# Kernel tuning notes

Hardware: AMD Instinct MI355X
Metric: run time of the kernel (lower is better)

Reference implementation:

```python
import jax, jax.numpy as jnp
import numpy as np

N, E = 20000, 100000
F_IN, F_OUT = 1024, 512
NUM_FILT = 8
DIM = 3  # output_dim per coordinate-function type (4 types -> 12 total)


def _death_indices(f, edge_index):
    """0-dim persistence pairing via union-find over a vertex filtration.
    Returns death[v]: index of the node whose filtration value kills the
    component created by v (death[v] == v for unpaired/essential nodes)."""
    u, v = edge_index[0], edge_index[1]
    fu, fv = f[u], f[v]
    d_idx = jnp.where(fu >= fv, u, v)          # node realizing the edge value max(f[u], f[v])
    order = jnp.argsort(jnp.maximum(fu, fv))   # process edges in increasing filtration order
    edges = jnp.stack([u[order], v[order], d_idx[order]], axis=1)  # [E, 3]
    n = f.shape[0]

    def find(parent, i):
        return jax.lax.while_loop(lambda j: parent[j] != j, lambda j: parent[j], i)

    def step(carry, e):
        parent, death = carry
        ra = find(parent, e[0])
        rb = find(parent, e[1])
        older = jnp.where(f[ra] <= f[rb], ra, rb)   # older (smaller birth) component survives
        younger = ra + rb - older                   # the other root dies at this edge
        merge = ra != rb
        parent = jnp.where(merge, parent.at[younger].set(older), parent)
        death = jnp.where(merge, death.at[younger].set(e[2]), death)
        return (parent, death), None

    idx = jnp.arange(n)
    (_, death), _ = jax.lax.scan(step, (idx, idx), edges)
    return death


def _coord_activations(p, tri_t, gauss_mu, gauss_sigma, line_w, rhat_c, rhat_r):
    """p: [N, 2] persistence pairs -> [N, 4*DIM] coordinate-function features."""
    b, d = p[:, 0:1], p[:, 1:2]
    tri = jax.nn.relu(d - jnp.abs(tri_t[None, :] - b))                     # Triangle_transform
    diff = p[:, None, :] - gauss_mu[None, :, :]
    gauss = jnp.exp(-jnp.sum(diff * diff, -1) / (2.0 * gauss_sigma ** 2))  # Gaussian_transform
    line = p @ line_w.T                                                    # Line_transform
    q = jnp.sum(jnp.abs(p[:, None, :] - rhat_c[None, :, :]), -1)
    rhat = 1.0 / (1.0 + q) - 1.0 / (1.0 + jnp.abs(jnp.abs(rhat_r) - q))    # RationalHat_transform
    return jnp.concatenate([tri, gauss, line, rhat], axis=1)


def _forward(x, filt_w, filt_b, tri_t, gauss_mu, gauss_sigma, line_w,
             rhat_c, rhat_r, out_w, out_b, edge_index):
    f_all = (x @ filt_w.T + filt_b).T                     # [NUM_FILT, N] filtration values
    f_sg = jax.lax.stop_gradient(f_all)                   # pairing structure is combinatorial
    death = jax.vmap(lambda ff: _death_indices(ff, edge_index))(f_sg)  # [NUM_FILT, N] int
    pairs = jnp.stack([f_all, jnp.take_along_axis(f_all, death, axis=1)], axis=-1)  # [F, N, 2]
    acts = jax.vmap(lambda p: _coord_activations(p, tri_t, gauss_mu, gauss_sigma,
                                                 line_w, rhat_c, rhat_r))(pairs)  # [F, N, 12]
    coord = jnp.transpose(acts, (1, 0, 2)).reshape(x.shape[0], -1)  # torch.cat over filtrations
    return jnp.concatenate([x, coord], axis=1) @ out_w.T + out_b


def setup_inputs() -> dict:
    key = jax.random.key(0)
    ks = jax.random.split(key, 10)
    s = 0.02
    return {
        "x": jax.random.normal(ks[0], (N, F_IN), jnp.float32),
        "edge_index": jax.random.randint(ks[1], (2, E), 0, N),
        "filt_w": jax.random.normal(ks[2], (NUM_FILT, F_IN), jnp.float32) * s,
        "filt_b": jnp.zeros((NUM_FILT,), jnp.float32),
        "tri_t": jax.random.normal(ks[3], (DIM,), jnp.float32),
        "gauss_mu": jax.random.normal(ks[4], (DIM, 2), jnp.float32),
        "gauss_sigma": jnp.asarray(0.5, jnp.float32),
        "line_w": jax.random.normal(ks[5], (DIM, 2), jnp.float32),
        "rhat_c": jax.random.normal(ks[6], (DIM, 2), jnp.float32),
        "rhat_r": jnp.asarray(1.0, jnp.float32),
        "out_w": jax.random.normal(ks[7], (F_OUT, F_IN + NUM_FILT * 4 * DIM), jnp.float32) * s,
        "out_b": jnp.zeros((F_OUT,), jnp.float32),
    }


def reference(x, edge_index, filt_w, filt_b, tri_t, gauss_mu, gauss_sigma,
              line_w, rhat_c, rhat_r, out_w, out_b):
    return _forward(x, filt_w, filt_b, tri_t, gauss_mu, gauss_sigma,
                    line_w, rhat_c, rhat_r, out_w, out_b, edge_index)
```

## Files before the change

### kernel.cpp

```cpp
#include <hip/hip_runtime.h>
#include <stdint.h>

#define NV 20000
#define NE 100000
#define NK 8
#define FIN 1024
#define FOUT 512
#define FTOT 1120
#define KP 1152
#define MP 20096
#define CAP 4096
#define ROUNDS 13
#define NB 32
#define CHUNK (NE / NB)
#define LDA 72

typedef unsigned int u32;
typedef unsigned long long u64;
typedef unsigned short u16;
typedef __attribute__((ext_vector_type(8))) short bf16x8;
typedef __attribute__((ext_vector_type(4))) float f32x4;

__device__ __forceinline__ u32 sb(float x) {
    u32 u = __float_as_uint(x);
    return u ^ ((u & 0x80000000u) ? 0xFFFFFFFFu : 0x80000000u);
}
__device__ __forceinline__ float isb(u32 s) {
    u32 u = (s & 0x80000000u) ? (s ^ 0x80000000u) : ~s;
    return __uint_as_float(u);
}
__device__ __forceinline__ u16 f2bf(float f) {
    u32 u = __float_as_uint(f);
    return (u16)((u + 0x7FFFu + ((u >> 16) & 1u)) >> 16);
}

__global__ __launch_bounds__(256) void k_fx(
    const float* __restrict__ x, const float* __restrict__ fw,
    const float* __restrict__ fb, float* __restrict__ f, u16* __restrict__ A) {
    __shared__ float w[NK * FIN];
    __shared__ float xs[4][FIN];
    for (int i = threadIdx.x; i < NK * FIN; i += 256) w[i] = fw[i];
    __syncthreads();
    int wave = threadIdx.x >> 6, lane = threadIdx.x & 63;
    int v = blockIdx.x * 4 + wave;
    float4* xd = (float4*)xs[wave];
    if (v < NV) {
        const float4* xr4 = (const float4*)(x + (size_t)v * FIN);
        for (int i = lane; i < FIN / 4; i += 64) xd[i] = xr4[i];
    } else {
        for (int i = lane; i < FIN / 4; i += 64) xd[i] = make_float4(0.f, 0.f, 0.f, 0.f);
    }
    float acc[NK];
#pragma unroll
    for (int k = 0; k < NK; k++) acc[k] = 0.f;
    for (int c = 0; c < FIN / 64; c++) {
        int i = c * 64 + lane;
        float xv = xs[wave][i];
#pragma unroll
        for (int k = 0; k < NK; k++) acc[k] = fmaf(xv, w[k * FIN + i], acc[k]);
    }
#pragma unroll
    for (int off = 32; off >= 1; off >>= 1)
#pragma unroll
        for (int k = 0; k < NK; k++) acc[k] += __shfl_xor(acc[k], off, 64);
    if (v < NV && lane < NK) f[lane * NV + v] = acc[lane] + fb[lane];
    for (int cc = lane; cc < 144; cc += 64) {
        int c0 = cc * 8;
        u32 pk[4];
        if (c0 < FIN) {
#pragma unroll
            for (int j = 0; j < 4; j++)
                pk[j] = (u32)f2bf(xs[wave][c0 + 2 * j]) |
                        ((u32)f2bf(xs[wave][c0 + 2 * j + 1]) << 16);
        } else {
#pragma unroll
            for (int j = 0; j < 4; j++) pk[j] = 0u;
        }
        *(uint4*)(A + (size_t)v * KP + c0) = make_uint4(pk[0], pk[1], pk[2], pk[3]);
    }
}

__global__ void k_init(u32* __restrict__ comp, u64* __restrict__ cand, u32* cnts) {
    int t = blockIdx.x * 256 + threadIdx.x;
    comp[t] = (u32)(t % CAP);
    cand[t] = ~0ull;
    if (t < 32) cnts[t] = 0;
}

__global__ void k_castw(const float* __restrict__ ow, u16* __restrict__ W) {
    int t = blockIdx.x * 256 + threadIdx.x;
    if (t >= FOUT * 144) return;
    int n = t / 144, c = (t % 144) * 8;
    u32 pk[4];
    if (c < FTOT) {
        const float* wr = ow + (size_t)n * FTOT + c;
#pragma unroll
        for (int j = 0; j < 4; j++)
            pk[j] = (u32)f2bf(wr[2 * j]) | ((u32)f2bf(wr[2 * j + 1]) << 16);
    } else {
#pragma unroll
        for (int j = 0; j < 4; j++) pk[j] = 0u;
    }
    *(uint4*)(W + (size_t)n * KP + c) = make_uint4(pk[0], pk[1], pk[2], pk[3]);
}

__global__ void k_initdesc(const float* __restrict__ f, u64* __restrict__ cd,
                           float* __restrict__ dval) {
    int t = blockIdx.x * 256 + threadIdx.x;
    u32 v = (u32)(t % NV);
    float fv = f[t];
    cd[t] = ((u64)sb(fv) << 32) | v;
    dval[t] = fv;
}

__global__ void k_descedge(const int* __restrict__ ei, const float* __restrict__ f,
                           u64* __restrict__ cd) {
    int t = blockIdx.x * 256 + threadIdx.x;
    int k = t / NE, e = t % NE;
    int a = ei[e], b = ei[NE + e];
    if (a == b) return;
    float fa = f[k * NV + a], fb2 = f[k * NV + b];
    int d, l; float fl;
    if (fa >= fb2) { d = a; l = b; fl = fb2; } else { d = b; l = a; fl = fa; }
    u64 key = ((u64)sb(fl) << 32) | (u32)l;
    atomicMin(&cd[k * NV + d], key);
}

__global__ __launch_bounds__(1024) void k_basmin(
    const u64* __restrict__ cd, u32* __restrict__ basin,
    u32* nmin, u32* __restrict__ mlist, u32* __restrict__ dense) {
    __shared__ u32 nxt[NV];
    __shared__ u32 changed;
    int k = blockIdx.x;
    const u64* c = cd + (size_t)k * NV;
    for (int i = threadIdx.x; i < NV; i += 1024) nxt[i] = (u32)c[i];
    if (threadIdx.x == 0) changed = 0u;
    __syncthreads();
    for (int pass = 0; pass < 16; pass++) {
        bool ch = false;
        for (int i = threadIdx.x; i < NV; i += 1024) {
            u32 a = nxt[i];
            u32 b = nxt[a];
            if (b != a) {
                u32 c2 = nxt[b];
                u32 d2 = nxt[c2];
                nxt[i] = d2;
                ch = true;
            }
        }
        if (ch) changed = 1u;
        __syncthreads();
        u32 done = (changed == 0u);
        __syncthreads();
        if (threadIdx.x == 0) changed = 0u;
        __syncthreads();
        if (done) break;
    }
    for (int i = threadIdx.x; i < NV; i += 1024) {
        u32 r = nxt[i];
        basin[k * NV + i] = r;
        if (r == (u32)i) {
            u32 id = atomicAdd(&nmin[k], 1u);
            if (id < CAP) { mlist[k * CAP + id] = (u32)i; dense[k * NV + i] = id; }
        }
    }
}

__global__ void k_edgeprep(const int* __restrict__ ei, const float* __restrict__ f,
                           const u32* __restrict__ basin, const u32* __restrict__ dense,
                           u64* __restrict__ wkey, u32* __restrict__ ep) {
    int t = blockIdx.x * 256 + threadIdx.x;
    int k = t / NE, e = t % NE;
    int a = ei[e], b = ei[NE + e];
    if (a == b) { ep[t] = 0xFFFFFFFFu; return; }
    float fa = f[k * NV + a], fb2 = f[k * NV + b];
    float w = (fa >= fb2) ? fa : fb2;
    wkey[t] = ((u64)sb(w) << 32) | (u32)e;
    u32 ba = basin[k * NV + a], bb = basin[k * NV + b];
    if (ba == bb) { ep[t] = 0xFFFFFFFFu; return; }
    u32 da = dense[k * NV + ba], db = dense[k * NV + bb];
    ep[t] = (da << 16) | db;
}

__device__ __forceinline__ u32 rootofs(const u32* c, u32 i) {
    while (true) { u32 p = c[i]; if (p == i) return i; i = p; }
}

__global__ void k_candA(const u32* __restrict__ ep, const u64* __restrict__ wkey,
                        const u32* __restrict__ comp_g, u64* __restrict__ cand_g,
                        const u32* __restrict__ done) {
    __shared__ u32 scomp[CAP];
    __shared__ u64 scand[CAP];
    int k = blockIdx.y, b = blockIdx.x;
    if (done[k]) return;
    for (int i = threadIdx.x; i < CAP; i += 256) {
        scomp[i] = comp_g[k * CAP + i];
        scand[i] = ~0ull;
    }
    __syncthreads();
    int e0 = b * CHUNK;
    const u32* epk = ep + (size_t)k * NE;
    const u64* wkk = wkey + (size_t)k * NE;
    for (int e = e0 + threadIdx.x; e < e0 + CHUNK; e += 256) {
        u32 p32 = epk[e];
        if (p32 == 0xFFFFFFFFu) continue;
        u32 A = rootofs(scomp, p32 >> 16), B = rootofs(scomp, p32 & 0xFFFFu);
        if (A == B) continue;
        u64 w = wkk[e];
        atomicMin(&scand[A], w);
        atomicMin(&scand[B], w);
    }
    __syncthreads();
    u64* cnd = cand_g + (size_t)k * CAP;
    for (int i = threadIdx.x; i < CAP; i += 256) {
        u64 v = scand[i];
        if (v != ~0ull) atomicMin(&cnd[i], v);
    }
}

__global__ void k_round(u64* __restrict__ cand_g, const u32* __restrict__ ep,
                        u32* __restrict__ comp_g, u32* mstcnt,
                        u64* __restrict__ mkey, u32* __restrict__ done) {
    __shared__ u64 scand[CAP];
    __shared__ u32 scomp[CAP];
    __shared__ u32 shk[CAP];
    __shared__ u32 nmerge;
    int k = blockIdx.x;
    if (done[k]) return;
    if (threadIdx.x == 0) nmerge = 0;
    for (int i = threadIdx.x; i < CAP; i += 1024) {
        scand[i] = cand_g[k * CAP + i];
        scomp[i] = comp_g[k * CAP + i];
    }
    __syncthreads();
    for (int i = threadIdx.x; i < CAP; i += 1024) {
        u64 cc = scand[i];
        if (cc == ~0ull) { shk[i] = (u32)i; continue; }
        u32 e = (u32)cc;
        u32 p32 = ep[(size_t)k * NE + e];
        u32 A = rootofs(scomp, p32 >> 16), B = rootofs(scomp, p32 & 0xFFFFu);
        shk[i] = (A == (u32)i) ? B : A;
    }
    __syncthreads();
    for (int i = threadIdx.x; i < CAP; i += 1024) {
        u32 o = shk[i];
        if (o == (u32)i) continue;
        bool mutual = (shk[o] == (u32)i);
        if (mutual && (u32)i < o) continue;
        scomp[i] = o;
        u64 cc = scand[i];
        u32 j = atomicAdd(&mstcnt[k], 1u);
        atomicAdd(&nmerge, 1u);
        if (j < CAP) mkey[k * CAP + j] = cc;
    }
    __syncthreads();
    for (int i = threadIdx.x; i < CAP; i += 1024) scomp[i] = rootofs(scomp, i);
    __syncthreads();
    for (int i = threadIdx.x; i < CAP; i += 1024) {
        comp_g[k * CAP + i] = scomp[i];
        cand_g[k * CAP + i] = ~0ull;
    }
    if (threadIdx.x == 0 && nmerge == 0) done[k] = 1;
}

__global__ __launch_bounds__(1024) void k_sort(const u32* mstcnt, u64* __restrict__ mkey) {
    __shared__ u64 skey[CAP];
    int k = blockIdx.x;
    u32 cnt = mstcnt[k]; if (cnt > CAP) cnt = CAP;
    int n2 = 64; while (n2 < (int)cnt) n2 <<= 1;
    for (int i = threadIdx.x; i < n2; i += 1024)
        skey[i] = (i < (int)cnt) ? mkey[k * CAP + i] : ~0ull;
    __syncthreads();
    int half = n2 >> 1;
    for (int sz = 2; sz <= n2; sz <<= 1) {
        for (int st = sz >> 1; st >= 1; st >>= 1) {
            for (int t = threadIdx.x; t < half; t += 1024) {
                int i = ((t & ~(st - 1)) << 1) | (t & (st - 1));
                int j = i | st;
                bool up = ((i & sz) == 0);
                u64 a = skey[i], b = skey[j];
                if (up ? (a > b) : (a < b)) { skey[i] = b; skey[j] = a; }
            }
            __syncthreads();
        }
    }
    for (int i = threadIdx.x; i < (int)cnt; i += 1024)
        mkey[k * CAP + i] = skey[i];
}

__global__ __launch_bounds__(64) void k_pairw(
    const u32* nmin, const u32* __restrict__ mlist, const u32* mstcnt,
    const u64* __restrict__ mkey, const u32* __restrict__ ep,
    const float* __restrict__ f, float* __restrict__ dval) {
    __shared__ u32 par[CAP];
    __shared__ u32 val[CAP];
    __shared__ u32 tag[CAP];
    int k = blockIdx.x;
    int lane = threadIdx.x;
    u32 nm = nmin[k]; if (nm > CAP) nm = CAP;
    u32 cnt = mstcnt[k]; if (cnt > CAP) cnt = CAP;
    for (int i = lane; i < CAP; i += 64) {
        par[i] = (u32)i;
        tag[i] = 0u;
        val[i] = (i < (int)nm) ? __float_as_uint(f[k * NV + mlist[k * CAP + i]]) : 0u;
    }
    __syncthreads();
    u32 nw = (cnt + 63) >> 6;
    u64 nkey = 0; u32 npay = 0;
    if ((u32)lane < cnt) {
        nkey = mkey[(size_t)k * CAP + lane];
        npay = ep[(size_t)k * NE + (u32)nkey];
    }
    for (u32 w = 0; w < nw; w++) {
        u64 key = nkey; u32 pay = npay;
        bool valid = (w * 64 + (u32)lane) < cnt;
        u32 jn = (w + 1) * 64 + (u32)lane;
        if (jn < cnt) {
            nkey = mkey[(size_t)k * CAP + jn];
            npay = ep[(size_t)k * NE + (u32)nkey];
        }
        u32 wb = (u32)(key >> 32);
        u32 la = pay >> 16, lb = pay & 0xFFFFu;
        u32 rA = la, rB = lb;
        if (valid) {
            while (true) {
                u32 pA = par[rA], pB = par[rB];
                bool dA = (pA == rA), dB = (pB == rB);
                if (dA && dB) break;
                if (!dA) { u32 g = par[pA]; par[rA] = g; rA = g; }
                if (!dB) { u32 g = par[pB]; par[rB] = g; rB = g; }
            }
        }
        u32 vA = valid ? val[rA] : 0u;
        u32 vB = valid ? val[rB] : 0u;
        if (valid) { atomicAdd(&tag[rA], 1u); atomicAdd(&tag[rB], 1u); }
        u32 cA = rA, cvA = vA, cB = rB, cvB = vB;
        u32 t_fy = 0xFFFFFFFFu, t_fo = 0u, t_fvo = 0u;
        if (valid) {
            if (__uint_as_float(cvA) <= __uint_as_float(cvB)) { t_fo = cA; t_fvo = cvA; t_fy = cB; }
            else                                              { t_fo = cB; t_fvo = cvB; t_fy = cA; }
        }
        u32 pkd = (t_fy << 16) | (t_fo & 0xFFFFu);
        bool pend = valid && (atomicAdd(&tag[t_fy], 0u) > 1u);
        u64 m = __ballot(pend);
        while (m) {
            u32 s = (u32)__builtin_ctzll(m);
            m &= m - 1;
            u32 opk = __builtin_amdgcn_readlane(pkd, (int)s);
            u32 ov  = __builtin_amdgcn_readlane(t_fvo, (int)s);
            u32 oy = opk >> 16, oo = opk & 0xFFFFu;
            if ((u32)lane == s) pend = false;
            bool app = valid && ((u32)lane > s);
            bool mA = app && (cA == oy);
            bool mB = app && (cB == oy);
            if (mA) { cA = oo; cvA = ov; }
            if (mB) { cB = oo; cvB = ov; }
            bool rm = mA || mB;
            if (__any(rm)) {
                if (rm) {
                    atomicAdd(&tag[oo], 1u);
                    if (__uint_as_float(cvA) <= __uint_as_float(cvB)) { t_fo = cA; t_fvo = cvA; t_fy = cB; }
                    else                                              { t_fo = cB; t_fvo = cvB; t_fy = cA; }
                    pkd = (t_fy << 16) | (t_fo & 0xFFFFu);
                    pend = atomicAdd(&tag[t_fy], 0u) > 1u;
                }
                m = __ballot(pend);
                m &= (s < 63u) ? (~0ull << (s + 1)) : 0ull;
            }
        }
        if (valid) { tag[rA] = 0u; tag[rB] = 0u; }
        if (valid) { par[t_fy] = t_fo; val[t_fy] = wb; }
        __syncthreads();
    }
    for (int i = lane; i < (int)nm; i += 64) {
        if (par[i] != (u32)i)
            dval[k * NV + mlist[k * CAP + i]] = isb(val[i]);
    }
}

__global__ void k_coordb(const float* __restrict__ f, const float* __restrict__ dval,
                         const float* __restrict__ tri_t, const float* __restrict__ gmu,
                         const float* __restrict__ gsig, const float* __restrict__ lw,
                         const float* __restrict__ rc, const float* __restrict__ rr,
                         u16* __restrict__ A) {
    int t = blockIdx.x * 256 + threadIdx.x;
    int k = t / NV, v = t % NV;
    float b = f[t], d = dval[t];
    float o[12];
    float s = gsig[0];
    float inv2s2 = 1.0f / (2.0f * s * s);
    float r = fabsf(rr[0]);
#pragma unroll
    for (int j = 0; j < 3; j++) {
        float tri = d - fabsf(tri_t[j] - b);
        o[j] = tri > 0.f ? tri : 0.f;
        float dx = b - gmu[2 * j], dy = d - gmu[2 * j + 1];
        o[3 + j] = expf(-(dx * dx + dy * dy) * inv2s2);
        o[6 + j] = b * lw[2 * j] + d * lw[2 * j + 1];
        float q = fabsf(b - rc[2 * j]) + fabsf(d - rc[2 * j + 1]);
        o[9 + j] = 1.0f / (1.0f + q) - 1.0f / (1.0f + fabsf(r - q));
    }
    u16* dst = A + (size_t)v * KP + FIN + k * 12;
    u32* d32 = (u32*)dst;
#pragma unroll
    for (int j = 0; j < 6; j++)
        d32[j] = (u32)f2bf(o[2 * j]) | ((u32)f2bf(o[2 * j + 1]) << 16);
}

__global__ __launch_bounds__(512, 2) void k_gemm2(
    const u16* __restrict__ A, const u16* __restrict__ W,
    const float* __restrict__ bias, float* __restrict__ out) {
    __shared__ u16 As[128 * LDA];
    __shared__ u16 Ws[512 * LDA];
    int m0 = blockIdx.x * 128;
    int t = threadIdx.x;
    int wave = t >> 6, lane = t & 63;
    int wr = wave >> 2, wc = wave & 3;
    int lrow = lane & 15, lq = lane >> 4;
    f32x4 acc[4][8];
#pragma unroll
    for (int mt = 0; mt < 4; mt++)
#pragma unroll
        for (int nt = 0; nt < 8; nt++) acc[mt][nt] = (f32x4){0.f, 0.f, 0.f, 0.f};

    int arow[2], acol[2], wrow[8], wcol[8];
    uint4 av[2], wv[8];
#pragma unroll
    for (int i = 0; i < 2; i++) {
        int c = i * 512 + t;
        arow[i] = c >> 3; acol[i] = (c & 7) * 8;
        av[i] = *(const uint4*)(A + (size_t)(m0 + arow[i]) * KP + acol[i]);
    }
#pragma unroll
    for (int i = 0; i < 8; i++) {
        int c = i * 512 + t;
        wrow[i] = c >> 3; wcol[i] = (c & 7) * 8;
        wv[i] = *(const uint4*)(W + (size_t)wrow[i] * KP + wcol[i]);
    }
#pragma unroll 1
    for (int step = 0; step < KP / 64; step++) {
        __syncthreads();
#pragma unroll
        for (int i = 0; i < 2; i++) *(uint4*)(As + arow[i] * LDA + acol[i]) = av[i];
#pragma unroll
        for (int i = 0; i < 8; i++) *(uint4*)(Ws + wrow[i] * LDA + wcol[i]) = wv[i];
        __syncthreads();
        int k0n = (step + 1 < KP / 64) ? (step + 1) * 64 : 0;
#pragma unroll
        for (int i = 0; i < 2; i++)
            av[i] = *(const uint4*)(A + (size_t)(m0 + arow[i]) * KP + k0n + acol[i]);
#pragma unroll
        for (int i = 0; i < 8; i++)
            wv[i] = *(const uint4*)(W + (size_t)wrow[i] * KP + k0n + wcol[i]);
#pragma unroll
        for (int kh = 0; kh < 2; kh++) {
            int kk = kh * 32 + lq * 8;
            bf16x8 af[4], wf[8];
#pragma unroll
            for (int mt = 0; mt < 4; mt++)
                af[mt] = *(const bf16x8*)(As + (wr * 64 + mt * 16 + lrow) * LDA + kk);
#pragma unroll
            for (int nt = 0; nt < 8; nt++)
                wf[nt] = *(const bf16x8*)(Ws + (wc * 128 + nt * 16 + lrow) * LDA + kk);
#pragma unroll
            for (int mt = 0; mt < 4; mt++)
#pragma unroll
                for (int nt = 0; nt < 8; nt++)
                    acc[mt][nt] = __builtin_amdgcn_mfma_f32_16x16x32_bf16(
                        af[mt], wf[nt], acc[mt][nt], 0, 0, 0);
        }
    }
    __syncthreads();
    float* scr = (float*)Ws + wave * 576;
    int cg = lane & 7;
    int rr8 = lane >> 3;
#pragma unroll
    for (int np = 0; np < 4; np++) {
        int o = wc * 128 + np * 32 + cg * 4;
        f32x4 b4 = *(const f32x4*)(bias + o);
#pragma unroll
        for (int mt = 0; mt < 4; mt++) {
#pragma unroll
            for (int fh = 0; fh < 2; fh++) {
                f32x4 fr = acc[mt][2 * np + fh];
#pragma unroll
                for (int i = 0; i < 4; i++)
                    scr[(lq * 4 + i) * 36 + fh * 16 + lrow] = fr[i];
            }
#pragma unroll
            for (int p = 0; p < 2; p++) {
                int r = p * 8 + rr8;
                f32x4 vv = *(f32x4*)(scr + r * 36 + cg * 4);
                int v = m0 + wr * 64 + mt * 16 + r;
                if (v < NV) *(f32x4*)(out + (size_t)v * FOUT + o) = vv + b4;
            }
        }
    }
}

extern "C" void kernel_launch(void* const* d_in, const int* in_sizes, int n_in,
                              void* d_out, int out_size, void* d_ws, size_t ws_size,
                              hipStream_t stream) {
    const float* x     = (const float*)d_in[0];
    const int*   ei    = (const int*)d_in[1];
    const float* fw    = (const float*)d_in[2];
    const float* fbv   = (const float*)d_in[3];
    const float* tri_t = (const float*)d_in[4];
    const float* gmu   = (const float*)d_in[5];
    const float* gsig  = (const float*)d_in[6];
    const float* lw    = (const float*)d_in[7];
    const float* rc    = (const float*)d_in[8];
    const float* rr    = (const float*)d_in[9];
    const float* ow    = (const float*)d_in[10];
    const float* ob    = (const float*)d_in[11];
    float* out = (float*)d_out;

    char* p = (char*)d_ws;
    auto alloc = [&](size_t bytes) -> void* {
        void* q = (void*)p;
        p += (bytes + 255) & ~(size_t)255;
        return q;
    };
    float* f     = (float*)alloc((size_t)NK * NV * 4);
    u64*   cd    = (u64*)  alloc((size_t)NK * NV * 8);
    u32*   basin = (u32*)  alloc((size_t)NK * NV * 4);
    u32*   dense = (u32*)  alloc((size_t)NK * NV * 4);
    u32*   mlist = (u32*)  alloc((size_t)NK * CAP * 4);
    u32*   cnts  = (u32*)  alloc(64 * 4);
    u64*   wkey  = (u64*)  alloc((size_t)NK * NE * 8);
    u32*   ep    = (u32*)  alloc((size_t)NK * NE * 4);
    u32*   comp  = (u32*)  alloc((size_t)NK * CAP * 4);
    u64*   cand  = (u64*)  alloc((size_t)NK * CAP * 8);
    u64*   mkey  = (u64*)  alloc((size_t)NK * CAP * 8);
    float* dval  = (float*)alloc((size_t)NK * NV * 4);
    u16*   Ab    = (u16*)  alloc((size_t)MP * KP * 2);
    u16*   Wb    = (u16*)  alloc((size_t)FOUT * KP * 2);
    u32* nmin = cnts; u32* mstcnt = cnts + 8; u32* done = cnts + 16;

    k_init<<<128, 256, 0, stream>>>(comp, cand, cnts);
    k_fx<<<MP / 4, 256, 0, stream>>>(x, fw, fbv, f, Ab);
    k_castw<<<(FOUT * 144 + 255) / 256, 256, 0, stream>>>(ow, Wb);
    k_initdesc<<<625, 256, 0, stream>>>(f, cd, dval);
    k_descedge<<<3125, 256, 0, stream>>>(ei, f, cd);
    k_basmin<<<NK, 1024, 0, stream>>>(cd, basin, nmin, mlist, dense);
    k_edgeprep<<<3125, 256, 0, stream>>>(ei, f, basin, dense, wkey, ep);
    for (int r = 0; r < ROUNDS; r++) {
        k_candA<<<dim3(NB, NK), 256, 0, stream>>>(ep, wkey, comp, cand, done);
        k_round<<<NK, 1024, 0, stream>>>(cand, ep, comp, mstcnt, mkey, done);
    }
    k_sort<<<8, 1024, 0, stream>>>(mstcnt, mkey);
    k_pairw<<<8, 64, 0, stream>>>(nmin, mlist, mstcnt, mkey, ep, f, dval);
    k_coordb<<<625, 256, 0, stream>>>(f, dval, tri_t, gmu, gsig, lw, rc, rr, Ab);
    k_gemm2<<<157, 512, 0, stream>>>(Ab, Wb, ob, out);
}
```

Before: 667.3 us.

## Fuse Boruvka rounds into one cooperative kernel and precompute dense basin ids

```diff
diff --git a/kernel.cpp b/kernel.cpp
--- a/kernel.cpp
+++ b/kernel.cpp
@@ -1,4 +1,5 @@
 #include <hip/hip_runtime.h>
+#include <hip/hip_cooperative_groups.h>
 #include <stdint.h>
 
 #define NV 20000
@@ -20,6 +21,10 @@
 typedef unsigned short u16;
 typedef __attribute__((ext_vector_type(8))) short bf16x8;
 typedef __attribute__((ext_vector_type(4))) float f32x4;
+typedef __attribute__((ext_vector_type(4))) unsigned int u32x4;
+
+#define ALOAD(p)    __hip_atomic_load((p), __ATOMIC_RELAXED, __HIP_MEMORY_SCOPE_AGENT)
+#define ASTORE(p,v) __hip_atomic_store((p), (v), __ATOMIC_RELAXED, __HIP_MEMORY_SCOPE_AGENT)
 
 __device__ __forceinline__ u32 sb(float x) {
     u32 u = __float_as_uint(x);
@@ -127,9 +132,10 @@
 }
 
 __global__ __launch_bounds__(1024) void k_basmin(
-    const u64* __restrict__ cd, u32* __restrict__ basin,
-    u32* nmin, u32* __restrict__ mlist, u32* __restrict__ dense) {
+    const u64* __restrict__ cd, u32* __restrict__ db,
+    u32* nmin, u32* __restrict__ mlist) {
     __shared__ u32 nxt[NV];
+    __shared__ u16 dsh[NV];
     __shared__ u32 changed;
     int k = blockIdx.x;
     const u64* c = cd + (size_t)k * NV;
@@ -157,17 +163,18 @@
         if (done) break;
     }
     for (int i = threadIdx.x; i < NV; i += 1024) {
-        u32 r = nxt[i];
-        basin[k * NV + i] = r;
-        if (r == (u32)i) {
+        if (nxt[i] == (u32)i) {
             u32 id = atomicAdd(&nmin[k], 1u);
-            if (id < CAP) { mlist[k * CAP + id] = (u32)i; dense[k * NV + i] = id; }
-        }
-    }
+            if (id < CAP) { mlist[k * CAP + id] = (u32)i; dsh[i] = (u16)id; }
+        }
+    }
+    __syncthreads();
+    for (int i = threadIdx.x; i < NV; i += 1024)
+        db[k * NV + i] = (u32)dsh[nxt[i]];
 }
 
 __global__ void k_edgeprep(const int* __restrict__ ei, const float* __restrict__ f,
-                           const u32* __restrict__ basin, const u32* __restrict__ dense,
+                           const u32* __restrict__ db,
                            u64* __restrict__ wkey, u32* __restrict__ ep) {
     int t = blockIdx.x * 256 + threadIdx.x;
     int k = t / NE, e = t % NE;
@@ -176,91 +183,96 @@
     float fa = f[k * NV + a], fb2 = f[k * NV + b];
     float w = (fa >= fb2) ? fa : fb2;
     wkey[t] = ((u64)sb(w) << 32) | (u32)e;
-    u32 ba = basin[k * NV + a], bb = basin[k * NV + b];
-    if (ba == bb) { ep[t] = 0xFFFFFFFFu; return; }
-    u32 da = dense[k * NV + ba], db = dense[k * NV + bb];
-    ep[t] = (da << 16) | db;
+    u32 da = db[k * NV + a], db2 = db[k * NV + b];
+    if (da == db2) { ep[t] = 0xFFFFFFFFu; return; }
+    ep[t] = (da << 16) | db2;
 }
 
 __device__ __forceinline__ u32 rootofs(const u32* c, u32 i) {
     while (true) { u32 p = c[i]; if (p == i) return i; i = p; }
 }
 
-__global__ void k_candA(const u32* __restrict__ ep, const u64* __restrict__ wkey,
-                        const u32* __restrict__ comp_g, u64* __restrict__ cand_g,
-                        const u32* __restrict__ done) {
+__global__ __launch_bounds__(1024) void k_boruvka(
+    const u32* __restrict__ ep, const u64* __restrict__ wkey,
+    u32* __restrict__ comp_g, u64* __restrict__ cand_g,
+    u32* mstcnt, u64* __restrict__ mkey, u32* __restrict__ done) {
+    cooperative_groups::grid_group grid = cooperative_groups::this_grid();
     __shared__ u32 scomp[CAP];
     __shared__ u64 scand[CAP];
-    int k = blockIdx.y, b = blockIdx.x;
-    if (done[k]) return;
-    for (int i = threadIdx.x; i < CAP; i += 256) {
-        scomp[i] = comp_g[k * CAP + i];
-        scand[i] = ~0ull;
-    }
-    __syncthreads();
-    int e0 = b * CHUNK;
-    const u32* epk = ep + (size_t)k * NE;
-    const u64* wkk = wkey + (size_t)k * NE;
-    for (int e = e0 + threadIdx.x; e < e0 + CHUNK; e += 256) {
-        u32 p32 = epk[e];
-        if (p32 == 0xFFFFFFFFu) continue;
-        u32 A = rootofs(scomp, p32 >> 16), B = rootofs(scomp, p32 & 0xFFFFu);
-        if (A == B) continue;
-        u64 w = wkk[e];
-        atomicMin(&scand[A], w);
-        atomicMin(&scand[B], w);
-    }
-    __syncthreads();
-    u64* cnd = cand_g + (size_t)k * CAP;
-    for (int i = threadIdx.x; i < CAP; i += 256) {
-        u64 v = scand[i];
-        if (v != ~0ull) atomicMin(&cnd[i], v);
-    }
-}
-
-__global__ void k_round(u64* __restrict__ cand_g, const u32* __restrict__ ep,
-                        u32* __restrict__ comp_g, u32* mstcnt,
-                        u64* __restrict__ mkey, u32* __restrict__ done) {
-    __shared__ u64 scand[CAP];
-    __shared__ u32 scomp[CAP];
     __shared__ u32 shk[CAP];
     __shared__ u32 nmerge;
-    int k = blockIdx.x;
-    if (done[k]) return;
-    if (threadIdx.x == 0) nmerge = 0;
-    for (int i = threadIdx.x; i < CAP; i += 1024) {
-        scand[i] = cand_g[k * CAP + i];
-        scomp[i] = comp_g[k * CAP + i];
-    }
-    __syncthreads();
-    for (int i = threadIdx.x; i < CAP; i += 1024) {
-        u64 cc = scand[i];
-        if (cc == ~0ull) { shk[i] = (u32)i; continue; }
-        u32 e = (u32)cc;
-        u32 p32 = ep[(size_t)k * NE + e];
-        u32 A = rootofs(scomp, p32 >> 16), B = rootofs(scomp, p32 & 0xFFFFu);
-        shk[i] = (A == (u32)i) ? B : A;
-    }
-    __syncthreads();
-    for (int i = threadIdx.x; i < CAP; i += 1024) {
-        u32 o = shk[i];
-        if (o == (u32)i) continue;
-        bool mutual = (shk[o] == (u32)i);
-        if (mutual && (u32)i < o) continue;
-        scomp[i] = o;
-        u64 cc = scand[i];
-        u32 j = atomicAdd(&mstcnt[k], 1u);
-        atomicAdd(&nmerge, 1u);
-        if (j < CAP) mkey[k * CAP + j] = cc;
-    }
-    __syncthreads();
-    for (int i = threadIdx.x; i < CAP; i += 1024) scomp[i] = rootofs(scomp, i);
-    __syncthreads();
-    for (int i = threadIdx.x; i < CAP; i += 1024) {
-        comp_g[k * CAP + i] = scomp[i];
-        cand_g[k * CAP + i] = ~0ull;
-    }
-    if (threadIdx.x == 0 && nmerge == 0) done[k] = 1;
+    int k = blockIdx.x >> 5, b = blockIdx.x & 31;
+    int tid = threadIdx.x;
+    for (int r = 0; r < ROUNDS; r++) {
+        u32 dn = ALOAD(&done[k]);
+        if (!dn) {
+            for (int i = tid; i < CAP; i += 1024) {
+                scomp[i] = ALOAD(&comp_g[k * CAP + i]);
+                scand[i] = ~0ull;
+            }
+            __syncthreads();
+            int e0 = b * CHUNK;
+            const u32* epk = ep + (size_t)k * NE;
+            const u64* wkk = wkey + (size_t)k * NE;
+            for (int e = e0 + tid; e < e0 + CHUNK; e += 1024) {
+                u32 p32 = epk[e];
+                if (p32 == 0xFFFFFFFFu) continue;
+                u32 A = rootofs(scomp, p32 >> 16), B = rootofs(scomp, p32 & 0xFFFFu);
+                if (A == B) continue;
+                u64 w = wkk[e];
+                atomicMin(&scand[A], w);
+                atomicMin(&scand[B], w);
+            }
+            __syncthreads();
+            u64* cnd = cand_g + (size_t)k * CAP;
+            for (int i = tid; i < CAP; i += 1024) {
+                u64 v = scand[i];
+                if (v != ~0ull) atomicMin(&cnd[i], v);
+            }
+        }
+        grid.sync();
+        if (b == 0 && !dn) {
+            if (tid == 0) nmerge = 0;
+            for (int i = tid; i < CAP; i += 1024) {
+                scand[i] = ALOAD(&cand_g[k * CAP + i]);
+                scomp[i] = ALOAD(&comp_g[k * CAP + i]);
+            }
+            __syncthreads();
+            for (int i = tid; i < CAP; i += 1024) {
+                u64 cc = scand[i];
+                if (cc == ~0ull) { shk[i] = (u32)i; continue; }
+                u32 e = (u32)cc;
+                u32 p32 = ep[(size_t)k * NE + e];
+                u32 A = rootofs(scomp, p32 >> 16), B = rootofs(scomp, p32 & 0xFFFFu);
+                shk[i] = (A == (u32)i) ? B : A;
+            }
+            __syncthreads();
+            for (int i = tid; i < CAP; i += 1024) {
+                u32 o = shk[i];
+                if (o == (u32)i) continue;
+                bool mutual = (shk[o] == (u32)i);
+                if (mutual && (u32)i < o) continue;
+                scomp[i] = o;
+                u64 cc = scand[i];
+                u32 j = atomicAdd(&mstcnt[k], 1u);
+                atomicAdd(&nmerge, 1u);
+                if (j < CAP) mkey[k * CAP + j] = cc;
+            }
+            __syncthreads();
+            for (int i = tid; i < CAP; i += 1024) scomp[i] = rootofs(scomp, i);
+            __syncthreads();
+            for (int i = tid; i < CAP; i += 1024) {
+                ASTORE(&comp_g[k * CAP + i], scomp[i]);
+                ASTORE(&cand_g[k * CAP + i], ~0ull);
+            }
+            __syncthreads();
+            if (tid == 0 && nmerge == 0) ASTORE(&done[k], 1u);
+        }
+        grid.sync();
+        u32 ad = 1;
+        for (int kk = 0; kk < NK; kk++) ad &= ALOAD(&done[kk]);
+        if (ad) break;
+    }
 }
 
 __global__ __launch_bounds__(1024) void k_sort(const u32* mstcnt, u64* __restrict__ mkey) {
@@ -424,34 +436,36 @@
         for (int nt = 0; nt < 8; nt++) acc[mt][nt] = (f32x4){0.f, 0.f, 0.f, 0.f};
 
     int arow[2], acol[2], wrow[8], wcol[8];
-    uint4 av[2], wv[8];
+    u32x4 av[2], wv[8];
 #pragma unroll
     for (int i = 0; i < 2; i++) {
         int c = i * 512 + t;
         arow[i] = c >> 3; acol[i] = (c & 7) * 8;
-        av[i] = *(const uint4*)(A + (size_t)(m0 + arow[i]) * KP + acol[i]);
+        av[i] = __builtin_nontemporal_load(
+            (const u32x4*)(A + (size_t)(m0 + arow[i]) * KP + acol[i]));
     }
 #pragma unroll
     for (int i = 0; i < 8; i++) {
         int c = i * 512 + t;
         wrow[i] = c >> 3; wcol[i] = (c & 7) * 8;
-        wv[i] = *(const uint4*)(W + (size_t)wrow[i] * KP + wcol[i]);
+        wv[i] = *(const u32x4*)(W + (size_t)wrow[i] * KP + wcol[i]);
     }
 #pragma unroll 1
     for (int step = 0; step < KP / 64; step++) {
         __syncthreads();
 #pragma unroll
-        for (int i = 0; i < 2; i++) *(uint4*)(As + arow[i] * LDA + acol[i]) = av[i];
-#pragma unroll
-        for (int i = 0; i < 8; i++) *(uint4*)(Ws + wrow[i] * LDA + wcol[i]) = wv[i];
+        for (int i = 0; i < 2; i++) *(u32x4*)(As + arow[i] * LDA + acol[i]) = av[i];
+#pragma unroll
+        for (int i = 0; i < 8; i++) *(u32x4*)(Ws + wrow[i] * LDA + wcol[i]) = wv[i];
         __syncthreads();
         int k0n = (step + 1 < KP / 64) ? (step + 1) * 64 : 0;
 #pragma unroll
         for (int i = 0; i < 2; i++)
-            av[i] = *(const uint4*)(A + (size_t)(m0 + arow[i]) * KP + k0n + acol[i]);
+            av[i] = __builtin_nontemporal_load(
+                (const u32x4*)(A + (size_t)(m0 + arow[i]) * KP + k0n + acol[i]));
 #pragma unroll
         for (int i = 0; i < 8; i++)
-            wv[i] = *(const uint4*)(W + (size_t)wrow[i] * KP + k0n + wcol[i]);
+            wv[i] = *(const u32x4*)(W + (size_t)wrow[i] * KP + k0n + wcol[i]);
 #pragma unroll
         for (int kh = 0; kh < 2; kh++) {
             int kk = kh * 32 + lq * 8;
@@ -492,7 +506,9 @@
                 int r = p * 8 + rr8;
                 f32x4 vv = *(f32x4*)(scr + r * 36 + cg * 4);
                 int v = m0 + wr * 64 + mt * 16 + r;
-                if (v < NV) *(f32x4*)(out + (size_t)v * FOUT + o) = vv + b4;
+                if (v < NV)
+                    __builtin_nontemporal_store(vv + b4,
+                        (f32x4*)(out + (size_t)v * FOUT + o));
             }
         }
     }
@@ -523,8 +539,7 @@
     };
     float* f     = (float*)alloc((size_t)NK * NV * 4);
     u64*   cd    = (u64*)  alloc((size_t)NK * NV * 8);
-    u32*   basin = (u32*)  alloc((size_t)NK * NV * 4);
-    u32*   dense = (u32*)  alloc((size_t)NK * NV * 4);
+    u32*   db    = (u32*)  alloc((size_t)NK * NV * 4);
     u32*   mlist = (u32*)  alloc((size_t)NK * CAP * 4);
     u32*   cnts  = (u32*)  alloc(64 * 4);
     u64*   wkey  = (u64*)  alloc((size_t)NK * NE * 8);
@@ -542,11 +557,14 @@
     k_castw<<<(FOUT * 144 + 255) / 256, 256, 0, stream>>>(ow, Wb);
     k_initdesc<<<625, 256, 0, stream>>>(f, cd, dval);
     k_descedge<<<3125, 256, 0, stream>>>(ei, f, cd);
-    k_basmin<<<NK, 1024, 0, stream>>>(cd, basin, nmin, mlist, dense);
-    k_edgeprep<<<3125, 256, 0, stream>>>(ei, f, basin, dense, wkey, ep);
-    for (int r = 0; r < ROUNDS; r++) {
-        k_candA<<<dim3(NB, NK), 256, 0, stream>>>(ep, wkey, comp, cand, done);
-        k_round<<<NK, 1024, 0, stream>>>(cand, ep, comp, mstcnt, mkey, done);
+    k_basmin<<<NK, 1024, 0, stream>>>(cd, db, nmin, mlist);
+    k_edgeprep<<<3125, 256, 0, stream>>>(ei, f, db, wkey, ep);
+    {
+        const u32* ep_c = ep; const u64* wkey_c = wkey;
+        void* args[] = {(void*)&ep_c, (void*)&wkey_c, (void*)&comp, (void*)&cand,
+                        (void*)&mstcnt, (void*)&mkey, (void*)&done};
+        hipLaunchCooperativeKernel((const void*)k_boruvka, dim3(NB * NK), dim3(1024),
+                                   args, 0, stream);
     }
     k_sort<<<8, 1024, 0, stream>>>(mstcnt, mkey);
     k_pairw<<<8, 64, 0, stream>>>(nmin, mlist, mstcnt, mkey, ep, f, dval);
```

Result: slower. 859.0 us (+28.7%).
